# Optimization experiments

Measured on AMD Instinct MI355X. Metric: run time of the kernel, lower is better.

The kernel has to match this reference:

```python
import jax, jax.numpy as jnp
import numpy as np

S = 16        # neighbor samples per layer
NL = 2        # number of GNN layers


def setup_inputs() -> dict:
    key = jax.random.key(0)
    ks = jax.random.split(key, 12)
    N_NODES, D, E, NMP, DEG, N_EDGE, B, NC = 50000, 128, 32, 3, 32, 200000, 1024, 8
    sc = 0.05
    return {
        "ids": jax.random.randint(ks[0], (B,), 0, N_NODES, dtype=jnp.int32),
        "feats": jax.random.normal(ks[1], (N_NODES, D), jnp.float32),
        "edge_emb": jax.random.normal(ks[2], (NMP, N_EDGE, E), jnp.float32),
        "adj_nodes": jax.random.randint(ks[3], (NMP, N_NODES, DEG), 0, N_NODES, dtype=jnp.int32),
        "adj_edges": jax.random.randint(ks[4], (NMP, N_NODES, DEG), 0, N_EDGE, dtype=jnp.int32),
        "W_self": jax.random.normal(ks[5], (NMP, NL, D, D), jnp.float32) * sc,
        "W_neigh": jax.random.normal(ks[6], (NMP, NL, D + E, D), jnp.float32) * sc,
        "W_edge": jax.random.normal(ks[7], (NMP, NL, 2 * D + E, E), jnp.float32) * sc,
        "attn": jax.random.normal(ks[8], (D,), jnp.float32) * sc,
        "fc_w": jax.random.normal(ks[9], (D, NC), jnp.float32) * sc,
        "fc_b": jnp.zeros((NC,), jnp.float32),
    }


def reference(ids, feats, edge_emb, adj_nodes, adj_edges, W_self, W_neigh, W_edge, attn, fc_w, fc_b):
    NMP = adj_nodes.shape[0]
    outs = []
    for mp in range(NMP):
        # --- sample neighbor tree (deterministic: first S columns) ---
        cur = ids
        all_feats = [feats[cur]]
        all_edges = []
        for _ in range(NL):
            nb = adj_nodes[mp][cur][:, :S].reshape(-1)     # [N*S]
            eid = adj_edges[mp][cur][:, :S].reshape(-1)    # [N*S]
            all_edges.append(edge_emb[mp][eid])            # [N*S, E]
            cur = nb
            all_feats.append(feats[cur])
        # --- per-layer aggregation + edge update ---
        for l in range(NL):
            new_feats = []
            for k in range(len(all_feats) - 1):
                xs, xn, ee = all_feats[k], all_feats[k + 1], all_edges[k]
                N = xs.shape[0]
                # mean over sampled neighbors of [neigh_feat || edge_emb]
                nin = jnp.concatenate(
                    [xn.reshape(N, S, -1), ee.reshape(N, S, -1)], axis=-1
                ).mean(axis=1)                             # [N, D+E]
                new_feats.append(jax.nn.relu(xs @ W_self[mp, l] + nin @ W_neigh[mp, l]))
            all_feats = new_feats  # dropout is identity in eval mode
            new_edges = []
            for k in range(len(all_edges) - 1):
                xs, xn, ee = all_feats[k], all_feats[k + 1], all_edges[k]
                rep = jnp.repeat(xs, S, axis=0)            # [N*S, D]
                new_edges.append(jax.nn.relu(
                    jnp.concatenate([rep, xn, ee], axis=-1) @ W_edge[mp, l]))
            all_edges = new_edges
        outs.append(all_feats[0])                          # [B, D]
    stacked = jnp.stack(outs)                              # [NMP, B, D]
    # metapath attention fuse
    scores = jnp.tanh(jnp.einsum('mbd,d->mb', stacked, attn))
    beta = jax.nn.softmax(scores, axis=0)
    emb = jnp.einsum('mb,mbd->bd', beta, stacked)          # [B, D]
    # F.normalize(dim=1)
    emb = emb / jnp.maximum(jnp.linalg.norm(emb, axis=1, keepdims=True), 1e-12)
    return emb @ fc_w + fc_b
```

## Files before the change

### kernel.cpp

```cpp
#include <hip/hip_runtime.h>

#define NNODES  50000
#define D       128
#define E       32
#define NMP     3
#define DEG     32
#define NEDGE   200000
#define B       1024
#define NC      8
#define S       16

#define RPM      17408
#define NKT      9
#define WSTRIDE  36864
#define WESTRIDE 9216

#define CONV_TASKS (1600000 + 6 * WSTRIDE + 3 * WESTRIDE)
#define TOT_TASKS  (CONV_TASKS + 3 * RPM)

typedef float f4 __attribute__((ext_vector_type(4)));
typedef short bh8 __attribute__((ext_vector_type(8)));

static __device__ __forceinline__ unsigned short f2bf(float f) {
    unsigned int u = __float_as_uint(f);
    u = u + 0x7FFFu + ((u >> 16) & 1u);
    return (unsigned short)(u >> 16);
}
static __device__ __forceinline__ float bf2f(unsigned short h) {
    return __uint_as_float(((unsigned int)h) << 16);
}

__global__ __launch_bounds__(256) void convsamp_k(
    const float* __restrict__ feats, const float* __restrict__ Ws,
    const float* __restrict__ Wn, const float* __restrict__ We,
    const int* __restrict__ ids, const int* __restrict__ adjn,
    const int* __restrict__ adje,
    unsigned short* __restrict__ fb, unsigned short* __restrict__ WT0,
    unsigned short* __restrict__ WTe, int* __restrict__ gx, int* __restrict__ eid1)
{
    int i = blockIdx.x * 256 + threadIdx.x;
    if (i < 1600000) {
        float4 v = ((const float4*)feats)[i];
        unsigned int p0 = (unsigned int)f2bf(v.x) | ((unsigned int)f2bf(v.y) << 16);
        unsigned int p1 = (unsigned int)f2bf(v.z) | ((unsigned int)f2bf(v.w) << 16);
        ((uint2*)fb)[i] = make_uint2(p0, p1);
    } else if (i < 1600000 + 6 * WSTRIDE) {
        int i2 = i - 1600000;
        int ml = i2 / WSTRIDE, e = i2 % WSTRIDE;
        int j = e & 7, t1 = e >> 3;
        int n = t1 & 127, t2 = t1 >> 7;
        int q = t2 & 3, kt = t2 >> 2;
        int k = kt * 32 + q * 8 + j;
        float v = (k < 128) ? Ws[((size_t)ml * 128 + k) * 128 + n]
                            : Wn[((size_t)ml * 160 + (k - 128)) * 128 + n];
        WT0[(size_t)ml * WSTRIDE + e] = f2bf(v);
    } else if (i < CONV_TASKS) {
        int i3 = i - 1600000 - 6 * WSTRIDE;
        int mp = i3 / WESTRIDE, e = i3 % WESTRIDE;
        int j = e & 7, t1 = e >> 3;
        int n = t1 & 31, t2 = t1 >> 5;
        int q = t2 & 3, kt = t2 >> 2;
        int k = kt * 32 + q * 8 + j;
        float v = We[(((size_t)mp * 2) * 288 + k) * 32 + n];
        WTe[(size_t)mp * WESTRIDE + e] = f2bf(v);
    } else if (i < TOT_TASKS) {
        int i4 = i - CONV_TASKS;
        int mp = i4 / RPM, r = i4 % RPM;
        if (r < 16384) {
            int node = ids[r >> 4];
            gx[mp * RPM + r]     = adjn[((size_t)mp * NNODES + node) * DEG + (r & 15)];
            eid1[mp * 16384 + r] = adje[((size_t)mp * NNODES + node) * DEG + (r & 15)];
        } else {
            gx[mp * RPM + r] = ids[r - 16384];
        }
    }
}

__global__ __launch_bounds__(256) void aggfeat_k(
    const unsigned short* __restrict__ fb, const float* __restrict__ edge_emb,
    const int* __restrict__ adjn, const int* __restrict__ adje,
    const int* __restrict__ gx, const int* __restrict__ eid1,
    const unsigned short* __restrict__ WT0,
    unsigned short* __restrict__ fout)
{
    __shared__ unsigned short Asm[32][136];
    __shared__ unsigned short Nsm[32][168];
    const int mp = blockIdx.y;
    const int w = threadIdx.x >> 6, t = threadIdx.x & 63;
    const int r0 = blockIdx.x * 32;
    const float* ee = edge_emb + (size_t)mp * NEDGE * E;
    const int hi = t >> 5, t31 = t & 31;
    const float inv = 1.0f / (float)S;

    for (int rr = 0; rr < 8; ++rr) {
        const int lr = w * 8 + rr;
        const int r = r0 + lr;
        const int self = __builtin_amdgcn_readfirstlane(gx[mp * RPM + r]);
        const int* ip;
        const int* eix;
        if (r < 16384) {
            ip  = adjn + ((size_t)mp * NNODES + self) * DEG;
            eix = adje + ((size_t)mp * NNODES + self) * DEG;
        } else {
            ip  = gx + mp * RPM + (r - 16384) * S;
            eix = eid1 + mp * 16384 + (r - 16384) * S;
        }
        unsigned int av = ((const unsigned int*)fb)[(size_t)self * 64 + t];
        unsigned int fv[S];
#pragma unroll
        for (int j = 0; j < S; ++j) {
            int nb = __builtin_amdgcn_readfirstlane(ip[j]);
            fv[j] = ((const unsigned int*)fb)[(size_t)nb * 64 + t];
        }
        float ev[S / 2];
#pragma unroll
        for (int e = 0; e < S / 2; ++e) {
            int e_ev = __builtin_amdgcn_readfirstlane(eix[2 * e]);
            int e_od = __builtin_amdgcn_readfirstlane(eix[2 * e + 1]);
            int edd = hi ? e_od : e_ev;
            ev[e] = ee[(size_t)edd * E + t31];
        }
        float s0 = 0.f, s1 = 0.f, se = 0.f;
#pragma unroll
        for (int j = 0; j < S; ++j) {
            s0 += bf2f((unsigned short)(fv[j] & 0xFFFF));
            s1 += bf2f((unsigned short)(fv[j] >> 16));
        }
#pragma unroll
        for (int e = 0; e < S / 2; ++e) se += ev[e];
        se += __shfl_xor(se, 32);

        ((unsigned int*)&Asm[lr][0])[t] = av;
        ((unsigned int*)&Nsm[lr][0])[t] =
            (unsigned int)f2bf(s0 * inv) | ((unsigned int)f2bf(s1 * inv) << 16);
        if (t < E) Nsm[lr][128 + t] = f2bf(se * inv);
    }
    __syncthreads();

    const int q = t >> 4, lm = t & 15;
    const unsigned short* wb = WT0 + (size_t)mp * 2 * WSTRIDE;

    f4 acc[2][2];
#pragma unroll
    for (int mt = 0; mt < 2; ++mt) { acc[mt][0] = (f4){0,0,0,0}; acc[mt][1] = (f4){0,0,0,0}; }

#pragma unroll
    for (int kt = 0; kt < NKT; ++kt) {
        const int k0 = kt * 32 + q * 8;
        bh8 a[2];
#pragma unroll
        for (int mt = 0; mt < 2; ++mt) {
            int lr = mt * 16 + lm;
            a[mt] = (k0 < 128) ? *(const bh8*)&Asm[lr][k0]
                               : *(const bh8*)&Nsm[lr][k0 - 128];
        }
        const unsigned short* wrow = wb + ((size_t)(kt * 4 + q) * 128 + lm) * 8;
#pragma unroll
        for (int ntl = 0; ntl < 2; ++ntl) {
            bh8 bf = *(const bh8*)(wrow + (w * 2 + ntl) * 16 * 8);
#pragma unroll
            for (int mt = 0; mt < 2; ++mt)
                acc[mt][ntl] = __builtin_amdgcn_mfma_f32_16x16x32_bf16(a[mt], bf, acc[mt][ntl], 0, 0, 0);
        }
    }

#pragma unroll
    for (int mt = 0; mt < 2; ++mt)
#pragma unroll
        for (int ntl = 0; ntl < 2; ++ntl)
#pragma unroll
            for (int rr = 0; rr < 4; ++rr) {
                int row = r0 + mt * 16 + q * 4 + rr;
                int col = (w * 2 + ntl) * 16 + lm;
                fout[((size_t)mp * RPM + row) * 128 + col] = f2bf(fmaxf(acc[mt][ntl][rr], 0.f));
            }
}

__global__ __launch_bounds__(256) void edgeagg_k(
    const unsigned short* __restrict__ fout, const float* __restrict__ edge_emb,
    const int* __restrict__ eid1, const unsigned short* __restrict__ WTe,
    unsigned short* __restrict__ agg1)
{
    const int mp = blockIdx.y;
    const int w = threadIdx.x >> 6, l = threadIdx.x & 63;
    const int q = l >> 4, lm = l & 15;
    const int m0 = blockIdx.x * 128 + w * 32;
    const unsigned short* we = WTe + (size_t)mp * WESTRIDE;
    const unsigned short* f1base = fout + (size_t)mp * RPM * 128;
    const unsigned short* f0base = fout + ((size_t)mp * RPM + 16384) * 128;
    const float* ee = edge_emb + (size_t)mp * NEDGE * E;
    const float inv = 1.0f / (float)S;

    const unsigned short* a1p[2];
    const unsigned short* a0p[2];
    int eidL[2];
#pragma unroll
    for (int mt = 0; mt < 2; ++mt) {
        int row = m0 + mt * 16 + lm;
        a1p[mt] = f1base + (size_t)row * 128;
        a0p[mt] = f0base + (size_t)(row >> 4) * 128;
        eidL[mt] = eid1[mp * 16384 + row];
    }

    f4 acc[2][2];
#pragma unroll
    for (int mt = 0; mt < 2; ++mt) { acc[mt][0] = (f4){0,0,0,0}; acc[mt][1] = (f4){0,0,0,0}; }

#pragma unroll
    for (int kt = 0; kt < NKT; ++kt) {
        const int k0 = kt * 32 + q * 8;
        bh8 a[2];
#pragma unroll
        for (int mt = 0; mt < 2; ++mt) {
            if (kt < 4) {
                a[mt] = *(const bh8*)(a0p[mt] + k0);
            } else if (kt < 8) {
                a[mt] = *(const bh8*)(a1p[mt] + (k0 - 128));
            } else {
                const float* ep = ee + (size_t)eidL[mt] * E + q * 8;
                float4 v0 = *(const float4*)ep;
                float4 v1 = *(const float4*)(ep + 4);
                bh8 tv;
                tv[0] = (short)f2bf(v0.x); tv[1] = (short)f2bf(v0.y);
                tv[2] = (short)f2bf(v0.z); tv[3] = (short)f2bf(v0.w);
                tv[4] = (short)f2bf(v1.x); tv[5] = (short)f2bf(v1.y);
                tv[6] = (short)f2bf(v1.z); tv[7] = (short)f2bf(v1.w);
                a[mt] = tv;
            }
        }
        const unsigned short* wrow = we + ((size_t)(kt * 4 + q) * 32 + lm) * 8;
        bh8 b0 = *(const bh8*)(wrow);
        bh8 b1 = *(const bh8*)(wrow + 16 * 8);
#pragma unroll
        for (int mt = 0; mt < 2; ++mt) {
            acc[mt][0] = __builtin_amdgcn_mfma_f32_16x16x32_bf16(a[mt], b0, acc[mt][0], 0, 0, 0);
            acc[mt][1] = __builtin_amdgcn_mfma_f32_16x16x32_bf16(a[mt], b1, acc[mt][1], 0, 0, 0);
        }
    }

#pragma unroll
    for (int mt = 0; mt < 2; ++mt) {
        int seg = (m0 >> 4) + mt;
#pragma unroll
        for (int nt = 0; nt < 2; ++nt) {
            float ps = 0.f;
#pragma unroll
            for (int rr = 0; rr < 4; ++rr) ps += fmaxf(acc[mt][nt][rr], 0.f);
            ps += __shfl_xor(ps, 16);
            ps += __shfl_xor(ps, 32);
            if (l < 16)
                agg1[((size_t)mp * B + seg) * 160 + 128 + nt * 16 + lm] = f2bf(ps * inv);
        }
    }

#pragma unroll
    for (int mt = 0; mt < 2; ++mt) {
        int seg = (m0 >> 4) + mt;
        const unsigned short* fr = f1base + (size_t)seg * 16 * 128;
        float s0 = 0.f, s1 = 0.f;
#pragma unroll
        for (int j = 0; j < S; ++j) {
            unsigned int u = ((const unsigned int*)(fr + j * 128))[l];
            s0 += bf2f((unsigned short)(u & 0xFFFF));
            s1 += bf2f((unsigned short)(u >> 16));
        }
        ((unsigned int*)(agg1 + ((size_t)mp * B + seg) * 160))[l] =
            (unsigned int)f2bf(s0 * inv) | ((unsigned int)f2bf(s1 * inv) << 16);
    }
}

__global__ __launch_bounds__(256) void feat1fin_k(
    const unsigned short* __restrict__ fout, const unsigned short* __restrict__ agg1,
    const unsigned short* __restrict__ WT0,
    const float* __restrict__ attn, const float* __restrict__ fcw,
    const float* __restrict__ fcb, float* __restrict__ out)
{
    __shared__ float sbuf[NMP][32][132];
    const int w = threadIdx.x >> 6, l = threadIdx.x & 63;
    const int q = l >> 4, lm = l & 15;
    const int m0 = blockIdx.x * 32;

    for (int task = w; task < 6; task += 4) {
        const int mp = task >> 1, mt = task & 1;
        const int row = m0 + mt * 16 + lm;
        const unsigned short* ap = fout + ((size_t)mp * RPM + 16384 + row) * 128;
        const unsigned short* np = agg1 + ((size_t)mp * B + row) * 160;
        const unsigned short* wb = WT0 + ((size_t)mp * 2 + 1) * WSTRIDE;

        f4 acc[8];
#pragma unroll
        for (int nt = 0; nt < 8; ++nt) acc[nt] = (f4){0.f, 0.f, 0.f, 0.f};
#pragma unroll
        for (int kt = 0; kt < NKT; ++kt) {
            const int k0 = kt * 32 + q * 8;
            bh8 a = (k0 < 128) ? *(const bh8*)(ap + k0) : *(const bh8*)(np + (k0 - 128));
            const unsigned short* wrow = wb + ((size_t)(kt * 4 + q) * 128 + lm) * 8;
#pragma unroll
            for (int nt = 0; nt < 8; ++nt) {
                bh8 bf = *(const bh8*)(wrow + nt * 16 * 8);
                acc[nt] = __builtin_amdgcn_mfma_f32_16x16x32_bf16(a, bf, acc[nt], 0, 0, 0);
            }
        }
#pragma unroll
        for (int nt = 0; nt < 8; ++nt)
#pragma unroll
            for (int rr = 0; rr < 4; ++rr)
                sbuf[mp][mt * 16 + q * 4 + rr][nt * 16 + lm] = fmaxf(acc[nt][rr], 0.f);
    }
    __syncthreads();

    const int row = threadIdx.x >> 3;
    const int j = threadIdx.x & 7;
    const int d0 = j * 16;
    float sc[NMP];
#pragma unroll
    for (int mp = 0; mp < NMP; ++mp) {
        float p = 0.f;
#pragma unroll
        for (int d = 0; d < 16; ++d) p += sbuf[mp][row][d0 + d] * attn[d0 + d];
        p += __shfl_xor(p, 1); p += __shfl_xor(p, 2); p += __shfl_xor(p, 4);
        sc[mp] = tanhf(p);
    }
    float mx = fmaxf(sc[0], fmaxf(sc[1], sc[2]));
    float e0 = expf(sc[0] - mx), e1 = expf(sc[1] - mx), e2 = expf(sc[2] - mx);
    float isum = 1.f / (e0 + e1 + e2);
    float b0 = e0 * isum, b1 = e1 * isum, b2 = e2 * isum;

    float emb[16];
    float nn = 0.f;
#pragma unroll
    for (int d = 0; d < 16; ++d) {
        float v = b0 * sbuf[0][row][d0 + d] + b1 * sbuf[1][row][d0 + d]
                + b2 * sbuf[2][row][d0 + d];
        emb[d] = v;
        nn += v * v;
    }
    nn += __shfl_xor(nn, 1); nn += __shfl_xor(nn, 2); nn += __shfl_xor(nn, 4);
    float innorm = 1.f / fmaxf(sqrtf(nn), 1e-12f);
#pragma unroll
    for (int d = 0; d < 16; ++d) emb[d] *= innorm;

#pragma unroll
    for (int c = 0; c < NC; ++c) {
        float p = 0.f;
#pragma unroll
        for (int d = 0; d < 16; ++d) p += emb[d] * fcw[(d0 + d) * NC + c];
        p += __shfl_xor(p, 1); p += __shfl_xor(p, 2); p += __shfl_xor(p, 4);
        if (j == c) out[(size_t)(m0 + row) * NC + c] = p + fcb[c];
    }
}

extern "C" void kernel_launch(void* const* d_in, const int* in_sizes, int n_in,
                              void* d_out, int out_size, void* d_ws, size_t ws_size,
                              hipStream_t stream) {
    const int* ids        = (const int*)d_in[0];
    const float* feats    = (const float*)d_in[1];
    const float* edge_emb = (const float*)d_in[2];
    const int* adjn       = (const int*)d_in[3];
    const int* adje       = (const int*)d_in[4];
    const float* Ws       = (const float*)d_in[5];
    const float* Wn       = (const float*)d_in[6];
    const float* We       = (const float*)d_in[7];
    const float* attn     = (const float*)d_in[8];
    const float* fcw      = (const float*)d_in[9];
    const float* fcb      = (const float*)d_in[10];
    float* out = (float*)d_out;

    char* p = (char*)d_ws;
    unsigned short* WT0 = (unsigned short*)p; p += (size_t)6 * WSTRIDE * 2;
    unsigned short* WTe = (unsigned short*)p; p += (size_t)3 * WESTRIDE * 2;
    unsigned short* fb  = (unsigned short*)p; p += (size_t)NNODES * 128 * 2;
    int* gx   = (int*)p;                      p += (size_t)3 * RPM * 4;
    int* eid1 = (int*)p;                      p += (size_t)3 * 16384 * 4;
    unsigned short* fout = (unsigned short*)p; p += (size_t)3 * RPM * 128 * 2;
    unsigned short* agg1 = (unsigned short*)p; p += (size_t)3 * B * 160 * 2;

    convsamp_k<<<TOT_TASKS / 256, 256, 0, stream>>>(feats, Ws, Wn, We, ids, adjn, adje,
                                                    fb, WT0, WTe, gx, eid1);
    aggfeat_k<<<dim3(RPM / 32, 3), 256, 0, stream>>>(fb, edge_emb, adjn, adje, gx, eid1,
                                                     WT0, fout);
    edgeagg_k<<<dim3(128, 3), 256, 0, stream>>>(fout, edge_emb, eid1, WTe, agg1);
    feat1fin_k<<<32, 256, 0, stream>>>(fout, agg1, WT0, attn, fcw, fcb, out);
}
```

Before: 242.9 us.

## Halve aggfeat rows per block and gather two rows concurrently per wave

The aggregation kernel now handles 16 rows per block instead of 32, doubling the grid, and each wave gathers two rows at once, which raises memory-level parallelism in the gather phase. The MFMA stage shrinks to one M-tile per wave. The intent is to hide gather latency with more blocks and more outstanding loads per wave. In exchange, more weight B-fragments are reloaded per row and register pressure rises from the doubled gather arrays.

```diff
diff --git a/kernel.cpp b/kernel.cpp
--- a/kernel.cpp
+++ b/kernel.cpp
@@ -83,97 +83,116 @@
     const unsigned short* __restrict__ WT0,
     unsigned short* __restrict__ fout)
 {
-    __shared__ unsigned short Asm[32][136];
-    __shared__ unsigned short Nsm[32][168];
+    __shared__ unsigned short Asm[16][136];
+    __shared__ unsigned short Nsm[16][168];
     const int mp = blockIdx.y;
     const int w = threadIdx.x >> 6, t = threadIdx.x & 63;
-    const int r0 = blockIdx.x * 32;
+    const int r0 = blockIdx.x * 16;
     const float* ee = edge_emb + (size_t)mp * NEDGE * E;
     const int hi = t >> 5, t31 = t & 31;
     const float inv = 1.0f / (float)S;
-
-    for (int rr = 0; rr < 8; ++rr) {
-        const int lr = w * 8 + rr;
-        const int r = r0 + lr;
-        const int self = __builtin_amdgcn_readfirstlane(gx[mp * RPM + r]);
-        const int* ip;
-        const int* eix;
-        if (r < 16384) {
-            ip  = adjn + ((size_t)mp * NNODES + self) * DEG;
-            eix = adje + ((size_t)mp * NNODES + self) * DEG;
+    const unsigned int* fb32 = (const unsigned int*)fb;
+    const int lvl1 = (r0 < 16384);
+
+    for (int pp = 0; pp < 2; ++pp) {
+        const int lra = w * 4 + pp * 2, lrb = lra + 1;
+        const int ra = r0 + lra, rb = r0 + lrb;
+        const int sa = __builtin_amdgcn_readfirstlane(gx[mp * RPM + ra]);
+        const int sb = __builtin_amdgcn_readfirstlane(gx[mp * RPM + rb]);
+        const int *ipa, *eixa, *ipb, *eixb;
+        if (lvl1) {
+            ipa  = adjn + ((size_t)mp * NNODES + sa) * DEG;
+            eixa = adje + ((size_t)mp * NNODES + sa) * DEG;
+            ipb  = adjn + ((size_t)mp * NNODES + sb) * DEG;
+            eixb = adje + ((size_t)mp * NNODES + sb) * DEG;
         } else {
-            ip  = gx + mp * RPM + (r - 16384) * S;
-            eix = eid1 + mp * 16384 + (r - 16384) * S;
-        }
-        unsigned int av = ((const unsigned int*)fb)[(size_t)self * 64 + t];
-        unsigned int fv[S];
+            ipa  = gx + mp * RPM + (ra - 16384) * S;
+            eixa = eid1 + mp * 16384 + (ra - 16384) * S;
+            ipb  = gx + mp * RPM + (rb - 16384) * S;
+            eixb = eid1 + mp * 16384 + (rb - 16384) * S;
+        }
+        unsigned int ava = fb32[(size_t)sa * 64 + t];
+        unsigned int avb = fb32[(size_t)sb * 64 + t];
+        unsigned int fva[S], fvb[S];
 #pragma unroll
         for (int j = 0; j < S; ++j) {
-            int nb = __builtin_amdgcn_readfirstlane(ip[j]);
-            fv[j] = ((const unsigned int*)fb)[(size_t)nb * 64 + t];
-        }
-        float ev[S / 2];
+            int na = __builtin_amdgcn_readfirstlane(ipa[j]);
+            fva[j] = fb32[(size_t)na * 64 + t];
+        }
+#pragma unroll
+        for (int j = 0; j < S; ++j) {
+            int nb = __builtin_amdgcn_readfirstlane(ipb[j]);
+            fvb[j] = fb32[(size_t)nb * 64 + t];
+        }
+        float eva[S / 2], evb[S / 2];
 #pragma unroll
         for (int e = 0; e < S / 2; ++e) {
-            int e_ev = __builtin_amdgcn_readfirstlane(eix[2 * e]);
-            int e_od = __builtin_amdgcn_readfirstlane(eix[2 * e + 1]);
-            int edd = hi ? e_od : e_ev;
-            ev[e] = ee[(size_t)edd * E + t31];
-        }
-        float s0 = 0.f, s1 = 0.f, se = 0.f;
+            int a_ev = __builtin_amdgcn_readfirstlane(eixa[2 * e]);
+            int a_od = __builtin_amdgcn_readfirstlane(eixa[2 * e + 1]);
+            eva[e] = ee[(size_t)(hi ? a_od : a_ev) * E + t31];
+        }
+#pragma unroll
+        for (int e = 0; e < S / 2; ++e) {
+            int b_ev = __builtin_amdgcn_readfirstlane(eixb[2 * e]);
+            int b_od = __builtin_amdgcn_readfirstlane(eixb[2 * e + 1]);
+            evb[e] = ee[(size_t)(hi ? b_od : b_ev) * E + t31];
+        }
+
+        float sa0 = 0.f, sa1 = 0.f, sea = 0.f;
+        float sb0 = 0.f, sb1 = 0.f, seb = 0.f;
 #pragma unroll
         for (int j = 0; j < S; ++j) {
-            s0 += bf2f((unsigned short)(fv[j] & 0xFFFF));
-            s1 += bf2f((unsigned short)(fv[j] >> 16));
-        }
-#pragma unroll
-        for (int e = 0; e < S / 2; ++e) se += ev[e];
-        se += __shfl_xor(se, 32);
-
-        ((unsigned int*)&Asm[lr][0])[t] = av;
-        ((unsigned int*)&Nsm[lr][0])[t] =
-            (unsigned int)f2bf(s0 * inv) | ((unsigned int)f2bf(s1 * inv) << 16);
-        if (t < E) Nsm[lr][128 + t] = f2bf(se * inv);
+            sa0 += bf2f((unsigned short)(fva[j] & 0xFFFF));
+            sa1 += bf2f((unsigned short)(fva[j] >> 16));
+            sb0 += bf2f((unsigned short)(fvb[j] & 0xFFFF));
+            sb1 += bf2f((unsigned short)(fvb[j] >> 16));
+        }
+#pragma unroll
+        for (int e = 0; e < S / 2; ++e) { sea += eva[e]; seb += evb[e]; }
+        sea += __shfl_xor(sea, 32);
+        seb += __shfl_xor(seb, 32);
+
+        ((unsigned int*)&Asm[lra][0])[t] = ava;
+        ((unsigned int*)&Asm[lrb][0])[t] = avb;
+        ((unsigned int*)&Nsm[lra][0])[t] =
+            (unsigned int)f2bf(sa0 * inv) | ((unsigned int)f2bf(sa1 * inv) << 16);
+        ((unsigned int*)&Nsm[lrb][0])[t] =
+            (unsigned int)f2bf(sb0 * inv) | ((unsigned int)f2bf(sb1 * inv) << 16);
+        if (t < E) {
+            Nsm[lra][128 + t] = f2bf(sea * inv);
+            Nsm[lrb][128 + t] = f2bf(seb * inv);
+        }
     }
     __syncthreads();
 
     const int q = t >> 4, lm = t & 15;
     const unsigned short* wb = WT0 + (size_t)mp * 2 * WSTRIDE;
 
-    f4 acc[2][2];
-#pragma unroll
-    for (int mt = 0; mt < 2; ++mt) { acc[mt][0] = (f4){0,0,0,0}; acc[mt][1] = (f4){0,0,0,0}; }
+    f4 acc[2];
+    acc[0] = (f4){0.f, 0.f, 0.f, 0.f};
+    acc[1] = (f4){0.f, 0.f, 0.f, 0.f};
 
 #pragma unroll
     for (int kt = 0; kt < NKT; ++kt) {
         const int k0 = kt * 32 + q * 8;
-        bh8 a[2];
-#pragma unroll
-        for (int mt = 0; mt < 2; ++mt) {
-            int lr = mt * 16 + lm;
-            a[mt] = (k0 < 128) ? *(const bh8*)&Asm[lr][k0]
-                               : *(const bh8*)&Nsm[lr][k0 - 128];
-        }
+        bh8 a = (k0 < 128) ? *(const bh8*)&Asm[lm][k0]
+                           : *(const bh8*)&Nsm[lm][k0 - 128];
         const unsigned short* wrow = wb + ((size_t)(kt * 4 + q) * 128 + lm) * 8;
 #pragma unroll
         for (int ntl = 0; ntl < 2; ++ntl) {
             bh8 bf = *(const bh8*)(wrow + (w * 2 + ntl) * 16 * 8);
-#pragma unroll
-            for (int mt = 0; mt < 2; ++mt)
-                acc[mt][ntl] = __builtin_amdgcn_mfma_f32_16x16x32_bf16(a[mt], bf, acc[mt][ntl], 0, 0, 0);
-        }
-    }
-
-#pragma unroll
-    for (int mt = 0; mt < 2; ++mt)
-#pragma unroll
-        for (int ntl = 0; ntl < 2; ++ntl)
-#pragma unroll
-            for (int rr = 0; rr < 4; ++rr) {
-                int row = r0 + mt * 16 + q * 4 + rr;
-                int col = (w * 2 + ntl) * 16 + lm;
-                fout[((size_t)mp * RPM + row) * 128 + col] = f2bf(fmaxf(acc[mt][ntl][rr], 0.f));
-            }
+            acc[ntl] = __builtin_amdgcn_mfma_f32_16x16x32_bf16(a, bf, acc[ntl], 0, 0, 0);
+        }
+    }
+
+#pragma unroll
+    for (int ntl = 0; ntl < 2; ++ntl)
+#pragma unroll
+        for (int rr = 0; rr < 4; ++rr) {
+            int row = r0 + q * 4 + rr;
+            int col = (w * 2 + ntl) * 16 + lm;
+            fout[((size_t)mp * RPM + row) * 128 + col] = f2bf(fmaxf(acc[ntl][rr], 0.f));
+        }
 }
 
 __global__ __launch_bounds__(256) void edgeagg_k(
@@ -377,7 +396,7 @@
 
     convsamp_k<<<TOT_TASKS / 256, 256, 0, stream>>>(feats, Ws, Wn, We, ids, adjn, adje,
                                                     fb, WT0, WTe, gx, eid1);
-    aggfeat_k<<<dim3(RPM / 32, 3), 256, 0, stream>>>(fb, edge_emb, adjn, adje, gx, eid1,
+    aggfeat_k<<<dim3(RPM / 16, 3), 256, 0, stream>>>(fb, edge_emb, adjn, adje, gx, eid1,
                                                      WT0, fout);
     edgeagg_k<<<dim3(128, 3), 256, 0, stream>>>(fout, edge_emb, eid1, WTe, agg1);
     feat1fin_k<<<32, 256, 0, stream>>>(fout, agg1, WT0, attn, fcw, fcb, out);
```

Measured after the change: 242.0 us. About the same (-0.4%).
